# Kernel optimization log

Measured on AMD Instinct MI355X. Metric: run time of the kernel, lower is better.

## Reference

```python
import jax, jax.numpy as jnp
from jax import lax
import numpy as np

T = 64          # psum accumulation length (input elements per partial sum)
NBITS_ACC = 8   # accumulator bit width
Q = 2 ** (NBITS_ACC - 1)  # signed clip range [-Q, Q-1]


def _binarize(x):
    """sign() binarization with straight-through estimator (hardtanh grad)."""
    xc = jnp.clip(x, -1.0, 1.0)
    return xc + lax.stop_gradient(jnp.sign(x) - xc)


def _binconv3x3(x, w, stride=1):
    """Binarized 3x3 conv with digital partial-sum clipping.

    Both activations and weights are binarized to {-1,0,+1} via sign. The
    reduction over Cin*3*3 is split into chunks of T elements; each chunk's
    partial sum is saturated to the nbits_acc-bit signed accumulator range
    before being added to the running total (digital psum scheme).
    """
    xb = _binarize(x)
    wb = _binarize(w)
    O, C, KH, KW = w.shape
    # patches: [N, C*KH*KW, Ho, Wo], feature dim ordered (C, KH, KW)
    patches = lax.conv_general_dilated_patches(
        xb, (KH, KW), (stride, stride), ((1, 1), (1, 1)))
    N, R, Ho, Wo = patches.shape
    G = R // T  # number of psum chunks (2304 / 64 = 36)
    p = patches.reshape(N, G, T, Ho, Wo).transpose(1, 0, 2, 3, 4)  # [G,N,T,H,W]
    wr = wb.reshape(O, G, T).transpose(1, 0, 2)                    # [G,O,T]

    def step(acc, gt):
        pg, wg = gt
        ps = jnp.einsum('nthw,ot->nohw', pg, wg)   # chunk partial sum
        ps = jnp.clip(ps, -float(Q), float(Q - 1))  # accumulator saturation
        return acc + ps, None

    init = jnp.zeros((N, O, Ho, Wo), x.dtype)
    out, _ = lax.scan(step, init, (p, wr))
    return out


def _bn(x, gamma, beta, eps=1e-5):
    # training-mode BatchNorm2d: batch statistics over (N, H, W)
    m = x.mean((0, 2, 3), keepdims=True)
    v = ((x - m) ** 2).mean((0, 2, 3), keepdims=True)
    return (x - m) / jnp.sqrt(v + eps) * gamma[None, :, None, None] + beta[None, :, None, None]


def setup_inputs() -> dict:
    key = jax.random.key(0)
    ks = jax.random.split(key, 3)
    N, C, H, W = 32, 256, 28, 28
    x = jax.random.normal(ks[0], (N, C, H, W), dtype=jnp.float32)
    w1 = jax.random.normal(ks[1], (C, C, 3, 3), dtype=jnp.float32) * 0.05
    w2 = jax.random.normal(ks[2], (C, C, 3, 3), dtype=jnp.float32) * 0.05
    return {
        'x': x,
        'w1': w1,
        'bn1_gamma': jnp.ones((C,), jnp.float32),
        'bn1_beta': jnp.zeros((C,), jnp.float32),
        'w2': w2,
        'bn2_gamma': jnp.ones((C,), jnp.float32),
        'bn2_beta': jnp.zeros((C,), jnp.float32),
    }


def reference(x, w1, bn1_gamma, bn1_beta, w2, bn2_gamma, bn2_beta):
    residual = x
    out = _binconv3x3(x, w1, stride=1)
    out = _bn(out, bn1_gamma, bn1_beta)
    out = jnp.clip(out, -1.0, 1.0)          # Hardtanh
    out = _binconv3x3(out, w2, stride=1)
    out = out + residual                    # identity residual (no downsample)
    out = _bn(out, bn2_gamma, bn2_beta)     # do_bntan=True
    out = jnp.clip(out, -1.0, 1.0)          # Hardtanh
    return out
```

## Files before the change

kernel.cpp:

```cpp
#include <hip/hip_runtime.h>
#include <stdint.h>

typedef unsigned long long u64;

#define NN 32
#define CC 256
#define HH 28
#define WW 28
#define PP 784
#define NHW 25088
#define WPO 36

__global__ __launch_bounds__(256) void pack_x(const float* __restrict__ x, u64* __restrict__ xp) {
    int h = blockIdx.x, n = blockIdx.y;
    int tid = threadIdx.x, lane = tid & 63, g = tid >> 6;
    int c = tid;
    const float* px = x + (((size_t)n * CC + c) * PP) + h * WW;
    float vals[28];
#pragma unroll
    for (int k = 0; k < 7; ++k) ((float4*)vals)[k] = ((const float4*)px)[k];
    u64* dst = xp + ((size_t)n * PP + h * WW) * 4 + g;
#pragma unroll
    for (int i = 0; i < 28; ++i) {
        u64 m = __ballot(vals[i] > 0.0f);
        if (lane == 0) dst[(size_t)i * 4] = m;
    }
}

__global__ __launch_bounds__(256) void pack_wz(const float* __restrict__ w1, const float* __restrict__ w2,
                                               u64* __restrict__ wp1, u64* __restrict__ wp2,
                                               int* s1i, u64* s1q, double* s2s, double* s2q) {
    int o = blockIdx.x, which = blockIdx.y;
    int tid = threadIdx.x, lane = tid & 63, g = tid >> 6;
    if (o == 0 && which == 0) {
        s1i[tid] = 0; s1q[tid] = 0ull; s2s[tid] = 0.0; s2q[tid] = 0.0;
    }
    const float* w = which ? w2 : w1;
    u64* wp = which ? wp2 : wp1;
    const float* pw = w + ((size_t)o * CC + tid) * 9;
#pragma unroll
    for (int tap = 0; tap < 9; ++tap) {
        u64 m = __ballot(pw[tap] > 0.0f);
        if (lane == 0) wp[(size_t)o * WPO + tap * 4 + g] = m;
    }
}


#define POP4(acc, T, WB) \
    acc += __popcll(T[0] ^ wreg[(WB)+0]) + __popcll(T[1] ^ wreg[(WB)+1]) \
         + __popcll(T[2] ^ wreg[(WB)+2]) + __popcll(T[3] ^ wreg[(WB)+3]);

#define LOADROW(T, lrow, ccc) { \
    ulonglong2 u0 = *(const ulonglong2*)&lin[lrow][ccc][0]; \
    ulonglong2 u1 = *(const ulonglong2*)&lin[lrow][ccc][2]; \
    T[0] = u0.x; T[1] = u0.y; T[2] = u1.x; T[3] = u1.y; }

#define COLBODY(ccc, AP, AC, AN) { \
    u64 t0[4], t1[4], t2[4]; \
    LOADROW(t1, wid + 1, ccc) \
    if (rtop) { LOADROW(t0, wid, ccc) } \
    if (rbot) { LOADROW(t2, wid + 2, ccc) } \
    if (rtop) { POP4(AN, t0, 0)  POP4(AC, t0, 4)  POP4(AP, t0, 8)  } \
    POP4(AN, t1, 12) POP4(AC, t1, 16) POP4(AP, t1, 20) \
    if (rbot) { POP4(AN, t2, 24) POP4(AC, t2, 28) POP4(AP, t2, 32) } }

#define EMIT(emc, A) { \
    int K = ((emc) == 0 || (emc) == 27) ? bb2 : bb3; \
    int dot = K - 2 * (A); \
    *vptr = (short)dot; vptr += CC; \
    if (MODE == 0) { tsi += dot; tqi += dot * dot; } \
    else { float u = (float)dot + resrow[emc]; tsf += u; tqf = fmaf(u, u, tqf); } }

template<int MODE>
__global__ __launch_bounds__(256, 3) void binconv(
    const u64* __restrict__ xp, const u64* __restrict__ wp,
    short* __restrict__ vout, const float* __restrict__ xres,
    int* __restrict__ s_i, u64* __restrict__ s_q,
    double* __restrict__ s2s, double* __restrict__ s2q)
{
    __shared__ u64 lin[6][28][4];
    __shared__ double reds[4][64];
    __shared__ double redq[4][64];

    int tid = threadIdx.x, lane = tid & 63, wid = tid >> 6;
    int rt = blockIdx.x, ob = blockIdx.y, n = blockIdx.z;
    int r0 = rt * 4;
    int o = ob * 64 + lane;

    for (int idx = tid; idx < 6 * 56; idx += 256) {
        int row = idx / 56, off = idx % 56;
        int gr = r0 - 1 + row;
        if (gr >= 0 && gr < HH) {
            ulonglong2 t = *(const ulonglong2*)(xp + ((size_t)n * PP + gr * WW) * 4 + off * 2);
            *(ulonglong2*)((u64*)lin + row * 112 + off * 2) = t;
        }
    }

    u64 wreg[36];
    {
        const ulonglong2* wv = (const ulonglong2*)(wp + (size_t)o * WPO);
#pragma unroll
        for (int k = 0; k < 18; ++k) { ulonglong2 t = wv[k]; wreg[2*k] = t.x; wreg[2*k+1] = t.y; }
    }
    __syncthreads();

    int r = r0 + wid;
    const bool rtop = (r > 0), rbot = (r < HH - 1);
    const int nr = 1 + (int)rtop + (int)rbot;
    const int bb3 = 256 * nr * 3, bb2 = 256 * nr * 2;

    short* vptr = vout + ((size_t)n * PP + (size_t)r * WW) * CC + o;
    const float* resrow = (MODE == 1) ? (xres + ((size_t)n * CC + o) * PP + r * WW) : nullptr;

    int tsi = 0, tqi = 0; float tsf = 0.0f, tqf = 0.0f;
    int a = 0, b = 0, c = 0;

    {
        u64 t0[4], t1[4], t2[4];
        LOADROW(t1, wid + 1, 0)
        if (rtop) { LOADROW(t0, wid, 0) }
        if (rbot) { LOADROW(t2, wid + 2, 0) }
        if (rtop) { POP4(c, t0, 0)  POP4(b, t0, 4)  }
        POP4(c, t1, 12) POP4(b, t1, 16)
        if (rbot) { POP4(c, t2, 24) POP4(b, t2, 28) }
    }

#pragma unroll 1
    for (int m = 0; m < 9; ++m) {
        int cc = 3 * m + 1;
        COLBODY(cc,     b, c, a)  EMIT(cc - 1, b)  b = 0;
        COLBODY(cc + 1, c, a, b)  EMIT(cc,     c)  c = 0;
        COLBODY(cc + 2, a, b, c)  EMIT(cc + 1, a)  a = 0;
    }
    EMIT(27, b)

    reds[wid][lane] = (MODE == 0) ? (double)tsi : (double)tsf;
    redq[wid][lane] = (MODE == 0) ? (double)tqi : (double)tqf;
    __syncthreads();
    if (wid == 0) {
        double S = reds[0][lane] + reds[1][lane] + reds[2][lane] + reds[3][lane];
        double Q = redq[0][lane] + redq[1][lane] + redq[2][lane] + redq[3][lane];
        if (MODE == 0) {
            atomicAdd(&s_i[o], (int)S);
            atomicAdd(&s_q[o], (u64)Q);
        } else {
            atomicAdd(&s2s[o], S);
            atomicAdd(&s2q[o], Q);
        }
    }
}

__global__ __launch_bounds__(256) void repack(const short* __restrict__ v1,
                                              const int* __restrict__ s_i, const u64* __restrict__ s_q,
                                              const float* __restrict__ gamma, const float* __restrict__ beta,
                                              u64* __restrict__ xp2) {
    int pt = blockIdx.x, n = blockIdx.y;
    int tid = threadIdx.x, lane = tid & 63, g = tid >> 6;
    int c = tid;
    double mean = (double)s_i[c] * (1.0 / NHW);
    double msq  = (double)s_q[c] * (1.0 / NHW);
    double var  = msq - mean * mean;
    double istd = 1.0 / sqrt(var + 1e-5);
    double ad   = (double)gamma[c] * istd;
    float a = (float)ad;
    float b = (float)((double)beta[c] - mean * ad);
#pragma unroll
    for (int i = 0; i < 16; ++i) {
        int p = pt * 16 + i;
        int v = v1[((size_t)n * PP + p) * CC + c];
        u64 m = __ballot(fmaf(a, (float)v, b) > 0.0f);
        if (lane == 0) xp2[((size_t)n * PP + p) * 4 + g] = m;
    }
}

__global__ __launch_bounds__(256) void finalize(const short* __restrict__ v2, const float* __restrict__ x,
                                                const double* __restrict__ s2s, const double* __restrict__ s2q,
                                                const float* __restrict__ gamma, const float* __restrict__ beta,
                                                float* __restrict__ out) {
    __shared__ short t[64 * 66];
    __shared__ float scs[64], bis[64];
    int ct = blockIdx.x, pt = blockIdx.y, n = blockIdx.z;
    int p0 = pt * 64, c0 = ct * 64;
    int tid = threadIdx.x;
    if (tid < 64) {
        int c = c0 + tid;
        double mean = s2s[c] * (1.0 / NHW);
        double msq  = s2q[c] * (1.0 / NHW);
        double var  = msq - mean * mean;
        double istd = 1.0 / sqrt(var + 1e-5);
        double ad   = (double)gamma[c] * istd;
        scs[tid] = (float)ad;
        bis[tid] = (float)((double)beta[c] - mean * ad);
    }
    for (int idx = tid; idx < 64 * 64; idx += 256) {
        int i = idx >> 6, j = idx & 63;
        int p = p0 + i;
        if (p < PP) t[i * 66 + j] = v2[((size_t)n * PP + p) * CC + c0 + j];
    }
    __syncthreads();
    int pl = tid & 63;
    int p = p0 + pl;
    if (p < PP) {
        for (int cl = tid >> 6; cl < 64; cl += 4) {
            int c = c0 + cl;
            float val = (float)t[pl * 66 + cl] + x[((size_t)n * CC + c) * PP + p];
            float r = fmaf(scs[cl], val, bis[cl]);
            r = fminf(fmaxf(r, -1.0f), 1.0f);
            out[((size_t)n * CC + c) * PP + p] = r;
        }
    }
}

extern "C" void kernel_launch(void* const* d_in, const int* in_sizes, int n_in,
                              void* d_out, int out_size, void* d_ws, size_t ws_size,
                              hipStream_t stream) {
    (void)in_sizes; (void)n_in; (void)out_size; (void)ws_size;
    const float* x   = (const float*)d_in[0];
    const float* w1  = (const float*)d_in[1];
    const float* g1  = (const float*)d_in[2];
    const float* b1  = (const float*)d_in[3];
    const float* w2  = (const float*)d_in[4];
    const float* g2  = (const float*)d_in[5];
    const float* b2  = (const float*)d_in[6];
    float* out = (float*)d_out;

    char* ws = (char*)d_ws;
    u64*    xp1 = (u64*)(ws + 0);
    u64*    xp2 = (u64*)(ws + 802816);
    u64*    wp1 = (u64*)(ws + 1605632);
    u64*    wp2 = (u64*)(ws + 1679360);
    int*    s1i = (int*)(ws + 1753088);
    u64*    s1q = (u64*)(ws + 1754112);
    double* s2s = (double*)(ws + 1756160);
    double* s2q = (double*)(ws + 1758208);
    short*  v12 = (short*)(ws + 1764352);

    pack_wz<<<dim3(256, 2), 256, 0, stream>>>(w1, w2, wp1, wp2, s1i, s1q, s2s, s2q);
    pack_x<<<dim3(28, 32), 256, 0, stream>>>(x, xp1);
    binconv<0><<<dim3(7, 4, 32), 256, 0, stream>>>(xp1, wp1, v12, nullptr, s1i, s1q, nullptr, nullptr);
    repack<<<dim3(49, 32), 256, 0, stream>>>(v12, s1i, s1q, g1, b1, xp2);
    binconv<1><<<dim3(7, 4, 32), 256, 0, stream>>>(xp2, wp2, v12, x, nullptr, nullptr, s2s, s2q);
    finalize<<<dim3(4, 13, 32), 256, 0, stream>>>(v12, x, s2s, s2q, g2, b2, out);
}
```

Measured before the change: 123.9 us.

## Compute two output rows per wave, fuse packing kernels, stage residual in LDS

Each wave in the binary conv now covers two adjacent output rows over half the columns, so each loaded middle input row is reused for both rows. This cuts LDS row loads per popcount. Mode 1 stages the residual tile in shared memory with a padded stride instead of strided global reads. The residual statistics are accumulated in double. The x and weight packing kernels are merged into one launch, and x packing switches from ballots to a per-thread bit loop over channels. The risks are more register pressure and a slower x-packing pattern.

Result: slower. 152.7 us (+23.2%).

```diff
diff --git a/kernel.cpp b/kernel.cpp
--- a/kernel.cpp
+++ b/kernel.cpp
@@ -11,76 +11,82 @@
 #define NHW 25088
 #define WPO 36
 
-__global__ __launch_bounds__(256) void pack_x(const float* __restrict__ x, u64* __restrict__ xp) {
-    int h = blockIdx.x, n = blockIdx.y;
-    int tid = threadIdx.x, lane = tid & 63, g = tid >> 6;
-    int c = tid;
-    const float* px = x + (((size_t)n * CC + c) * PP) + h * WW;
-    float vals[28];
+__global__ __launch_bounds__(64) void prep(const float* __restrict__ x,
+        const float* __restrict__ w1, const float* __restrict__ w2,
+        u64* __restrict__ xp, u64* __restrict__ wp1, u64* __restrict__ wp2,
+        int* s1i, u64* s1q, double* s2s, double* s2q) {
+    int bx = blockIdx.x, lane = threadIdx.x;
+    if (bx < 1664) {
+        int n = bx / 52, rem = bx % 52, g = rem / 13, pt = rem % 13;
+        int p = pt * 64 + lane;
+        if (p < PP) {
+            const float* base = x + ((size_t)n * CC + g * 64) * PP + p;
+            u64 w = 0;
+#pragma unroll 8
+            for (int cb = 0; cb < 64; ++cb)
+                if (base[(size_t)cb * PP] > 0.0f) w |= (1ull << cb);
+            xp[((size_t)n * PP + p) * 4 + g] = w;
+        }
+    } else {
+        int u = bx - 1664, which = u >> 8, o = u & 255;
+        if (u < 4) {
+            s1i[u * 64 + lane] = 0; s1q[u * 64 + lane] = 0ull;
+            s2s[u * 64 + lane] = 0.0; s2q[u * 64 + lane] = 0.0;
+        }
+        const float* w = which ? w2 : w1;
+        u64* wp = which ? wp2 : wp1;
 #pragma unroll
-    for (int k = 0; k < 7; ++k) ((float4*)vals)[k] = ((const float4*)px)[k];
-    u64* dst = xp + ((size_t)n * PP + h * WW) * 4 + g;
-#pragma unroll
-    for (int i = 0; i < 28; ++i) {
-        u64 m = __ballot(vals[i] > 0.0f);
-        if (lane == 0) dst[(size_t)i * 4] = m;
-    }
-}
-
-__global__ __launch_bounds__(256) void pack_wz(const float* __restrict__ w1, const float* __restrict__ w2,
-                                               u64* __restrict__ wp1, u64* __restrict__ wp2,
-                                               int* s1i, u64* s1q, double* s2s, double* s2q) {
-    int o = blockIdx.x, which = blockIdx.y;
-    int tid = threadIdx.x, lane = tid & 63, g = tid >> 6;
-    if (o == 0 && which == 0) {
-        s1i[tid] = 0; s1q[tid] = 0ull; s2s[tid] = 0.0; s2q[tid] = 0.0;
-    }
-    const float* w = which ? w2 : w1;
-    u64* wp = which ? wp2 : wp1;
-    const float* pw = w + ((size_t)o * CC + tid) * 9;
-#pragma unroll
-    for (int tap = 0; tap < 9; ++tap) {
-        u64 m = __ballot(pw[tap] > 0.0f);
-        if (lane == 0) wp[(size_t)o * WPO + tap * 4 + g] = m;
-    }
-}
-
-
-#define POP4(acc, T, WB) \
-    acc += __popcll(T[0] ^ wreg[(WB)+0]) + __popcll(T[1] ^ wreg[(WB)+1]) \
-         + __popcll(T[2] ^ wreg[(WB)+2]) + __popcll(T[3] ^ wreg[(WB)+3]);
-
-#define LOADROW(T, lrow, ccc) { \
-    ulonglong2 u0 = *(const ulonglong2*)&lin[lrow][ccc][0]; \
-    ulonglong2 u1 = *(const ulonglong2*)&lin[lrow][ccc][2]; \
-    T[0] = u0.x; T[1] = u0.y; T[2] = u1.x; T[3] = u1.y; }
-
-#define COLBODY(ccc, AP, AC, AN) { \
-    u64 t0[4], t1[4], t2[4]; \
-    LOADROW(t1, wid + 1, ccc) \
-    if (rtop) { LOADROW(t0, wid, ccc) } \
-    if (rbot) { LOADROW(t2, wid + 2, ccc) } \
-    if (rtop) { POP4(AN, t0, 0)  POP4(AC, t0, 4)  POP4(AP, t0, 8)  } \
-    POP4(AN, t1, 12) POP4(AC, t1, 16) POP4(AP, t1, 20) \
-    if (rbot) { POP4(AN, t2, 24) POP4(AC, t2, 28) POP4(AP, t2, 32) } }
-
-#define EMIT(emc, A) { \
-    int K = ((emc) == 0 || (emc) == 27) ? bb2 : bb3; \
-    int dot = K - 2 * (A); \
-    *vptr = (short)dot; vptr += CC; \
-    if (MODE == 0) { tsi += dot; tqi += dot * dot; } \
-    else { float u = (float)dot + resrow[emc]; tsf += u; tqf = fmaf(u, u, tqf); } }
+        for (int cg = 0; cg < 4; ++cg)
+            for (int tap = 0; tap < 9; ++tap) {
+                u64 m = __ballot(w[((size_t)o * CC + cg * 64 + lane) * 9 + tap] > 0.0f);
+                if (lane == 0) wp[(size_t)o * WPO + tap * 4 + cg] = m;
+            }
+    }
+}
+
+
+#define POPW(acc, T, wb) acc = (int)__popcll((T) ^ wreg[wb]) + acc;
+#define POP4S(acc, T, WB) { POPW(acc, T##0, (WB)+0) POPW(acc, T##1, (WB)+1) \
+                            POPW(acc, T##2, (WB)+2) POPW(acc, T##3, (WB)+3) }
+
+#define LOADROW(T, lr, ccc) { \
+    ulonglong2 u0 = *(const ulonglong2*)&lin[lr][ccc][0]; \
+    ulonglong2 u1 = *(const ulonglong2*)&lin[lr][ccc][2]; \
+    T##0 = u0.x; T##1 = u0.y; T##2 = u1.x; T##3 = u1.y; }
+
+#define COLBODY2(ccc, PA,CA,NA, PB,CB,NB) { \
+    u64 t00,t01,t02,t03, t10,t11,t12,t13, t20,t21,t22,t23, t30,t31,t32,t33; \
+    LOADROW(t1, lw+1, ccc) LOADROW(t2, lw+2, ccc) \
+    if (rtopA) { LOADROW(t0, lw, ccc) } \
+    if (rbotB) { LOADROW(t3, lw+3, ccc) } \
+    if (rtopA) { POP4S(NA, t0, 0) POP4S(CA, t0, 4) POP4S(PA, t0, 8) } \
+    POP4S(NA, t1, 12) POP4S(CA, t1, 16) POP4S(PA, t1, 20) \
+    POP4S(NB, t1, 0)  POP4S(CB, t1, 4)  POP4S(PB, t1, 8)  \
+    POP4S(NA, t2, 24) POP4S(CA, t2, 28) POP4S(PA, t2, 32) \
+    POP4S(NB, t2, 12) POP4S(CB, t2, 16) POP4S(PB, t2, 20) \
+    if (rbotB) { POP4S(NB, t3, 24) POP4S(CB, t3, 28) POP4S(PB, t3, 32) } }
+
+#define EMIT2(e, AA, AB) { \
+    int nc = ((e) == 0 || (e) == 27) ? 2 : 3; \
+    int dA = kA * nc - 2 * (AA); int dB = kB * nc - 2 * (AB); \
+    vrowA[(size_t)(e) * CC] = (short)dA; vrowB[(size_t)(e) * CC] = (short)dB; \
+    if (MODE == 0) { tsi += dA + dB; tqi += dA * dA + dB * dB; } \
+    else { float uA = (float)dA + xt[xoffA + (e)]; \
+           float uB = (float)dB + xt[xoffA + 28 + (e)]; \
+           ts += (double)uA + (double)uB; \
+           tq += (double)uA * uA + (double)uB * uB; } }
 
 template<int MODE>
-__global__ __launch_bounds__(256, 3) void binconv(
-    const u64* __restrict__ xp, const u64* __restrict__ wp,
-    short* __restrict__ vout, const float* __restrict__ xres,
-    int* __restrict__ s_i, u64* __restrict__ s_q,
-    double* __restrict__ s2s, double* __restrict__ s2q)
+__global__ __attribute__((amdgpu_flat_work_group_size(256, 256), amdgpu_waves_per_eu(3, 3)))
+void binconv(const u64* __restrict__ xp, const u64* __restrict__ wp,
+             short* __restrict__ vout, const float* __restrict__ xres,
+             int* __restrict__ s_i, u64* __restrict__ s_q,
+             double* __restrict__ s2s, double* __restrict__ s2q)
 {
     __shared__ u64 lin[6][28][4];
-    __shared__ double reds[4][64];
-    __shared__ double redq[4][64];
+    __shared__ float xt[(MODE == 1) ? (64 * 113) : 1];
+    __shared__ int ris[(MODE == 0) ? 256 : 1], riq[(MODE == 0) ? 256 : 1];
+    __shared__ double rds[(MODE == 1) ? 256 : 1], rdq[(MODE == 1) ? 256 : 1];
 
     int tid = threadIdx.x, lane = tid & 63, wid = tid >> 6;
     int rt = blockIdx.x, ob = blockIdx.y, n = blockIdx.z;
@@ -95,6 +101,15 @@
             *(ulonglong2*)((u64*)lin + row * 112 + off * 2) = t;
         }
     }
+    if (MODE == 1) {
+        const float* xb = xres + ((size_t)n * CC + ob * 64) * PP + r0 * WW;
+        for (int idx = tid; idx < 1792; idx += 256) {
+            int f4 = idx % 7, row = (idx / 7) & 3, ch = idx / 28;
+            float4 v = *(const float4*)(xb + (size_t)ch * PP + row * WW + f4 * 4);
+            float* d = &xt[ch * 113 + row * 28 + f4 * 4];
+            d[0] = v.x; d[1] = v.y; d[2] = v.z; d[3] = v.w;
+        }
+    }
 
     u64 wreg[36];
     {
@@ -104,46 +119,48 @@
     }
     __syncthreads();
 
-    int r = r0 + wid;
-    const bool rtop = (r > 0), rbot = (r < HH - 1);
-    const int nr = 1 + (int)rtop + (int)rbot;
-    const int bb3 = 256 * nr * 3, bb2 = 256 * nr * 2;
-
-    short* vptr = vout + ((size_t)n * PP + (size_t)r * WW) * CC + o;
-    const float* resrow = (MODE == 1) ? (xres + ((size_t)n * CC + o) * PP + r * WW) : nullptr;
-
-    int tsi = 0, tqi = 0; float tsf = 0.0f, tqf = 0.0f;
-    int a = 0, b = 0, c = 0;
-
-    {
-        u64 t0[4], t1[4], t2[4];
-        LOADROW(t1, wid + 1, 0)
-        if (rtop) { LOADROW(t0, wid, 0) }
-        if (rbot) { LOADROW(t2, wid + 2, 0) }
-        if (rtop) { POP4(c, t0, 0)  POP4(b, t0, 4)  }
-        POP4(c, t1, 12) POP4(b, t1, 16)
-        if (rbot) { POP4(c, t2, 24) POP4(b, t2, 28) }
-    }
+    const int h = wid & 1, rp = wid >> 1;
+    const int lw = rp * 2;
+    const int rA = r0 + lw;
+    const bool rtopA = (rA > 0), rbotB = (rA + 1 < HH - 1);
+    const int kA = 256 * (2 + (rtopA ? 1 : 0));
+    const int kB = 256 * (2 + (rbotB ? 1 : 0));
+    const int c0 = 13 * h, emin = 14 * h;
+    const int xoffA = (MODE == 1) ? (lane * 113 + lw * 28) : 0;
+
+    short* vrowA = vout + ((size_t)n * PP + (size_t)rA * WW) * CC + o;
+    short* vrowB = vrowA + (size_t)WW * CC;
+
+    int tsi = 0, tqi = 0; double ts = 0.0, tq = 0.0;
+    int aA = 0, bA = 0, cA = 0, aB = 0, bB = 0, cB = 0;
 
 #pragma unroll 1
-    for (int m = 0; m < 9; ++m) {
-        int cc = 3 * m + 1;
-        COLBODY(cc,     b, c, a)  EMIT(cc - 1, b)  b = 0;
-        COLBODY(cc + 1, c, a, b)  EMIT(cc,     c)  c = 0;
-        COLBODY(cc + 2, a, b, c)  EMIT(cc + 1, a)  a = 0;
-    }
-    EMIT(27, b)
-
-    reds[wid][lane] = (MODE == 0) ? (double)tsi : (double)tsf;
-    redq[wid][lane] = (MODE == 0) ? (double)tqi : (double)tqf;
+    for (int t = 0; t < 5; ++t) {
+        int i0 = c0 + 3 * t;
+        COLBODY2(i0,     bA,cA,aA, bB,cB,aB)
+        if (i0 - 1 >= emin) { EMIT2(i0 - 1, bA, bB) }
+        bA = 0; bB = 0;
+        COLBODY2(i0 + 1, cA,aA,bA, cB,aB,bB)
+        if (i0 >= emin)     { EMIT2(i0,     cA, cB) }
+        cA = 0; cB = 0;
+        COLBODY2(i0 + 2, aA,bA,cA, aB,bB,cB)
+        if (i0 + 1 >= emin) { EMIT2(i0 + 1, aA, aB) }
+        aA = 0; aB = 0;
+    }
+    if (h == 1) { EMIT2(27, bA, bB) }
+
+    if (MODE == 0) { ris[wid * 64 + lane] = tsi; riq[wid * 64 + lane] = tqi; }
+    else           { rds[wid * 64 + lane] = ts;  rdq[wid * 64 + lane] = tq; }
     __syncthreads();
     if (wid == 0) {
-        double S = reds[0][lane] + reds[1][lane] + reds[2][lane] + reds[3][lane];
-        double Q = redq[0][lane] + redq[1][lane] + redq[2][lane] + redq[3][lane];
         if (MODE == 0) {
-            atomicAdd(&s_i[o], (int)S);
-            atomicAdd(&s_q[o], (u64)Q);
+            int S = ris[lane] + ris[64 + lane] + ris[128 + lane] + ris[192 + lane];
+            int Q = riq[lane] + riq[64 + lane] + riq[128 + lane] + riq[192 + lane];
+            atomicAdd(&s_i[o], S);
+            atomicAdd(&s_q[o], (u64)(long long)Q);
         } else {
+            double S = rds[lane] + rds[64 + lane] + rds[128 + lane] + rds[192 + lane];
+            double Q = rdq[lane] + rdq[64 + lane] + rdq[128 + lane] + rdq[192 + lane];
             atomicAdd(&s2s[o], S);
             atomicAdd(&s2q[o], Q);
         }
@@ -235,8 +252,7 @@
     double* s2q = (double*)(ws + 1758208);
     short*  v12 = (short*)(ws + 1764352);
 
-    pack_wz<<<dim3(256, 2), 256, 0, stream>>>(w1, w2, wp1, wp2, s1i, s1q, s2s, s2q);
-    pack_x<<<dim3(28, 32), 256, 0, stream>>>(x, xp1);
+    prep<<<2176, 64, 0, stream>>>(x, w1, w2, xp1, wp1, wp2, s1i, s1q, s2s, s2q);
     binconv<0><<<dim3(7, 4, 32), 256, 0, stream>>>(xp1, wp1, v12, nullptr, s1i, s1q, nullptr, nullptr);
     repack<<<dim3(49, 32), 256, 0, stream>>>(v12, s1i, s1q, g1, b1, xp2);
     binconv<1><<<dim3(7, 4, 32), 256, 0, stream>>>(xp2, wp2, v12, x, nullptr, nullptr, s2s, s2q);
```

## Merge packing kernels and shrink binconv blocks to two rows

Applied to the files above, without the earlier changes.

Folds the x-packing and weight-packing kernels into one prep launch. In prep, each thread builds a 64-channel bit mask by looping over channels instead of using wave ballots, which gives coalesced reads along the spatial dimension. The binconv kernels now use 128-thread blocks covering 2 rows each, so there are twice as many blocks and a smaller shared-memory halo per block, with occupancy hints set. Weight registers are pinned with empty asm constraints to keep them in VGPRs. The cost is a larger halo-load ratio (4 rows loaded per 2 computed) and a serial per-thread channel loop in prep.

Measured after the change: 123.7 us. No clear change (-0.2%).

```diff
diff --git a/kernel.cpp b/kernel.cpp
--- a/kernel.cpp
+++ b/kernel.cpp
@@ -11,48 +11,47 @@
 #define NHW 25088
 #define WPO 36
 
-__global__ __launch_bounds__(256) void pack_x(const float* __restrict__ x, u64* __restrict__ xp) {
-    int h = blockIdx.x, n = blockIdx.y;
-    int tid = threadIdx.x, lane = tid & 63, g = tid >> 6;
-    int c = tid;
-    const float* px = x + (((size_t)n * CC + c) * PP) + h * WW;
-    float vals[28];
+__global__ __launch_bounds__(64) void prep(const float* __restrict__ x,
+        const float* __restrict__ w1, const float* __restrict__ w2,
+        u64* __restrict__ xp, u64* __restrict__ wp1, u64* __restrict__ wp2,
+        int* s1i, u64* s1q, double* s2s, double* s2q) {
+    int bx = blockIdx.x, lane = threadIdx.x;
+    if (bx < 1664) {
+        int n = bx / 52, rem = bx % 52, g = rem / 13, pt = rem % 13;
+        int p = pt * 64 + lane;
+        if (p < PP) {
+            const float* base = x + ((size_t)n * CC + g * 64) * PP + p;
+            u64 w = 0;
+#pragma unroll 8
+            for (int cb = 0; cb < 64; ++cb)
+                if (base[(size_t)cb * PP] > 0.0f) w |= (1ull << cb);
+            xp[((size_t)n * PP + p) * 4 + g] = w;
+        }
+    } else {
+        int u = bx - 1664, which = u >> 8, o = u & 255;
+        if (u < 4) {
+            s1i[u * 64 + lane] = 0; s1q[u * 64 + lane] = 0ull;
+            s2s[u * 64 + lane] = 0.0; s2q[u * 64 + lane] = 0.0;
+        }
+        const float* w = which ? w2 : w1;
+        u64* wp = which ? wp2 : wp1;
 #pragma unroll
-    for (int k = 0; k < 7; ++k) ((float4*)vals)[k] = ((const float4*)px)[k];
-    u64* dst = xp + ((size_t)n * PP + h * WW) * 4 + g;
-#pragma unroll
-    for (int i = 0; i < 28; ++i) {
-        u64 m = __ballot(vals[i] > 0.0f);
-        if (lane == 0) dst[(size_t)i * 4] = m;
-    }
-}
-
-__global__ __launch_bounds__(256) void pack_wz(const float* __restrict__ w1, const float* __restrict__ w2,
-                                               u64* __restrict__ wp1, u64* __restrict__ wp2,
-                                               int* s1i, u64* s1q, double* s2s, double* s2q) {
-    int o = blockIdx.x, which = blockIdx.y;
-    int tid = threadIdx.x, lane = tid & 63, g = tid >> 6;
-    if (o == 0 && which == 0) {
-        s1i[tid] = 0; s1q[tid] = 0ull; s2s[tid] = 0.0; s2q[tid] = 0.0;
-    }
-    const float* w = which ? w2 : w1;
-    u64* wp = which ? wp2 : wp1;
-    const float* pw = w + ((size_t)o * CC + tid) * 9;
-#pragma unroll
-    for (int tap = 0; tap < 9; ++tap) {
-        u64 m = __ballot(pw[tap] > 0.0f);
-        if (lane == 0) wp[(size_t)o * WPO + tap * 4 + g] = m;
-    }
-}
-
-
-#define POP4(acc, T, WB) \
-    acc += __popcll(T[0] ^ wreg[(WB)+0]) + __popcll(T[1] ^ wreg[(WB)+1]) \
-         + __popcll(T[2] ^ wreg[(WB)+2]) + __popcll(T[3] ^ wreg[(WB)+3]);
-
-#define LOADROW(T, lrow, ccc) { \
-    ulonglong2 u0 = *(const ulonglong2*)&lin[lrow][ccc][0]; \
-    ulonglong2 u1 = *(const ulonglong2*)&lin[lrow][ccc][2]; \
+        for (int cg = 0; cg < 4; ++cg)
+            for (int tap = 0; tap < 9; ++tap) {
+                u64 m = __ballot(w[((size_t)o * CC + cg * 64 + lane) * 9 + tap] > 0.0f);
+                if (lane == 0) wp[(size_t)o * WPO + tap * 4 + cg] = m;
+            }
+    }
+}
+
+
+#define POPW(acc, T, wb) acc = (int)__popcll((T) ^ wreg[wb]) + acc;
+#define POP4(acc, T, WB) { POPW(acc, T[0], (WB)+0) POPW(acc, T[1], (WB)+1) \
+                           POPW(acc, T[2], (WB)+2) POPW(acc, T[3], (WB)+3) }
+
+#define LOADROW(T, lr, ccc) { \
+    ulonglong2 u0 = *(const ulonglong2*)&lin[lr][ccc][0]; \
+    ulonglong2 u1 = *(const ulonglong2*)&lin[lr][ccc][2]; \
     T[0] = u0.x; T[1] = u0.y; T[2] = u1.x; T[3] = u1.y; }
 
 #define COLBODY(ccc, AP, AC, AN) { \
@@ -72,22 +71,22 @@
     else { float u = (float)dot + resrow[emc]; tsf += u; tqf = fmaf(u, u, tqf); } }
 
 template<int MODE>
-__global__ __launch_bounds__(256, 3) void binconv(
-    const u64* __restrict__ xp, const u64* __restrict__ wp,
-    short* __restrict__ vout, const float* __restrict__ xres,
-    int* __restrict__ s_i, u64* __restrict__ s_q,
-    double* __restrict__ s2s, double* __restrict__ s2q)
+__global__ __attribute__((amdgpu_flat_work_group_size(128, 128), amdgpu_waves_per_eu(3, 4)))
+void binconv(const u64* __restrict__ xp, const u64* __restrict__ wp,
+             short* __restrict__ vout, const float* __restrict__ xres,
+             int* __restrict__ s_i, u64* __restrict__ s_q,
+             double* __restrict__ s2s, double* __restrict__ s2q)
 {
-    __shared__ u64 lin[6][28][4];
-    __shared__ double reds[4][64];
-    __shared__ double redq[4][64];
+    __shared__ u64 lin[4][28][4];
+    __shared__ double reds[2][64];
+    __shared__ double redq[2][64];
 
     int tid = threadIdx.x, lane = tid & 63, wid = tid >> 6;
     int rt = blockIdx.x, ob = blockIdx.y, n = blockIdx.z;
-    int r0 = rt * 4;
+    int r0 = rt * 2;
     int o = ob * 64 + lane;
 
-    for (int idx = tid; idx < 6 * 56; idx += 256) {
+    for (int idx = tid; idx < 4 * 56; idx += 128) {
         int row = idx / 56, off = idx % 56;
         int gr = r0 - 1 + row;
         if (gr >= 0 && gr < HH) {
@@ -102,6 +101,16 @@
 #pragma unroll
         for (int k = 0; k < 18; ++k) { ulonglong2 t = wv[k]; wreg[2*k] = t.x; wreg[2*k+1] = t.y; }
     }
+    asm volatile("" : "+v"(wreg[0]), "+v"(wreg[1]), "+v"(wreg[2]), "+v"(wreg[3]),
+                      "+v"(wreg[4]), "+v"(wreg[5]), "+v"(wreg[6]), "+v"(wreg[7]),
+                      "+v"(wreg[8]), "+v"(wreg[9]), "+v"(wreg[10]), "+v"(wreg[11]),
+                      "+v"(wreg[12]), "+v"(wreg[13]), "+v"(wreg[14]), "+v"(wreg[15]),
+                      "+v"(wreg[16]), "+v"(wreg[17]));
+    asm volatile("" : "+v"(wreg[18]), "+v"(wreg[19]), "+v"(wreg[20]), "+v"(wreg[21]),
+                      "+v"(wreg[22]), "+v"(wreg[23]), "+v"(wreg[24]), "+v"(wreg[25]),
+                      "+v"(wreg[26]), "+v"(wreg[27]), "+v"(wreg[28]), "+v"(wreg[29]),
+                      "+v"(wreg[30]), "+v"(wreg[31]), "+v"(wreg[32]), "+v"(wreg[33]),
+                      "+v"(wreg[34]), "+v"(wreg[35]));
     __syncthreads();
 
     int r = r0 + wid;
@@ -138,11 +147,11 @@
     redq[wid][lane] = (MODE == 0) ? (double)tqi : (double)tqf;
     __syncthreads();
     if (wid == 0) {
-        double S = reds[0][lane] + reds[1][lane] + reds[2][lane] + reds[3][lane];
-        double Q = redq[0][lane] + redq[1][lane] + redq[2][lane] + redq[3][lane];
+        double S = reds[0][lane] + reds[1][lane];
+        double Q = redq[0][lane] + redq[1][lane];
         if (MODE == 0) {
             atomicAdd(&s_i[o], (int)S);
-            atomicAdd(&s_q[o], (u64)Q);
+            atomicAdd(&s_q[o], (u64)(long long)Q);
         } else {
             atomicAdd(&s2s[o], S);
             atomicAdd(&s2q[o], Q);
@@ -235,10 +244,9 @@
     double* s2q = (double*)(ws + 1758208);
     short*  v12 = (short*)(ws + 1764352);
 
-    pack_wz<<<dim3(256, 2), 256, 0, stream>>>(w1, w2, wp1, wp2, s1i, s1q, s2s, s2q);
-    pack_x<<<dim3(28, 32), 256, 0, stream>>>(x, xp1);
-    binconv<0><<<dim3(7, 4, 32), 256, 0, stream>>>(xp1, wp1, v12, nullptr, s1i, s1q, nullptr, nullptr);
+    prep<<<2176, 64, 0, stream>>>(x, w1, w2, xp1, wp1, wp2, s1i, s1q, s2s, s2q);
+    binconv<0><<<dim3(14, 4, 32), 128, 0, stream>>>(xp1, wp1, v12, nullptr, s1i, s1q, nullptr, nullptr);
     repack<<<dim3(49, 32), 256, 0, stream>>>(v12, s1i, s1q, g1, b1, xp2);
-    binconv<1><<<dim3(7, 4, 32), 256, 0, stream>>>(xp2, wp2, v12, x, nullptr, nullptr, s2s, s2q);
+    binconv<1><<<dim3(14, 4, 32), 128, 0, stream>>>(xp2, wp2, v12, x, nullptr, nullptr, s2s, s2q);
     finalize<<<dim3(4, 13, 32), 256, 0, stream>>>(v12, x, s2s, s2q, g2, b2, out);
 }
```
